# Optimization experiments

Hardware: AMD Instinct MI355X
Metric: run time of the kernel (lower is better)

The kernel has to match this reference:

```python
import jax, jax.numpy as jnp
import numpy as np

FEAT_DIM = 128
GUIDE_DIM = 128
NIR_DIM = 32
H_LR, W_LR = 128, 128
H_HR, W_HR = 256, 256
IMNET_IN = FEAT_DIM + 2 * GUIDE_DIM + 2  # 386


def make_coord_1d(n):
    # pixel-center coords in [-1, 1]: (2i+1)/n - 1
    return (2.0 * jnp.arange(n, dtype=jnp.float32) + 1.0) / n - 1.0


def nearest_sample(img, cy, cx):
    """F.grid_sample(img, grid, mode='nearest', align_corners=False, padding='zeros').
    img: [b, C, h, w]; cy, cx: [N] normalized coords (cy -> h axis, cx -> w axis).
    Returns sampled values [b, C, N] and the pixel-center coords (qcy, qcx) the
    nearest sample corresponds to (0 when out of range, matching zero padding)."""
    h, w = img.shape[-2], img.shape[-1]
    iy = jnp.round(((cy + 1.0) * h - 1.0) * 0.5).astype(jnp.int32)  # round-half-even == nearbyint
    ix = jnp.round(((cx + 1.0) * w - 1.0) * 0.5).astype(jnp.int32)
    valid = (iy >= 0) & (iy < h) & (ix >= 0) & (ix < w)
    iyc = jnp.clip(iy, 0, h - 1)
    ixc = jnp.clip(ix, 0, w - 1)
    out = img[:, :, iyc, ixc]                       # [b, C, N] gather
    out = jnp.where(valid[None, None, :], out, 0.0)
    qcy = jnp.where(valid, (2.0 * iyc.astype(jnp.float32) + 1.0) / h - 1.0, 0.0)
    qcx = jnp.where(valid, (2.0 * ixc.astype(jnp.float32) + 1.0) / w - 1.0, 0.0)
    return out, qcy, qcx


def mlp(x, W1, b1, W2, b2, W3, b3):
    x = jax.nn.relu(x @ W1 + b1)
    x = jax.nn.relu(x @ W2 + b2)
    return x @ W3 + b3


def setup_inputs() -> dict:
    key = jax.random.key(0)
    ks = jax.random.split(key, 9)
    return {
        "feat": jax.random.normal(ks[0], (1, FEAT_DIM, H_LR, W_LR), jnp.float32),
        "lr_guide": jax.random.normal(ks[1], (1, GUIDE_DIM, H_LR, W_LR), jnp.float32),
        "hr_guide": jax.random.normal(ks[2], (1, GUIDE_DIM, H_HR, W_HR), jnp.float32),
        "W1": jax.random.normal(ks[3], (IMNET_IN, 256), jnp.float32) * 0.05,
        "b1": jax.random.normal(ks[4], (256,), jnp.float32) * 0.05,
        "W2": jax.random.normal(ks[5], (256, 128), jnp.float32) * 0.05,
        "b2": jax.random.normal(ks[6], (128,), jnp.float32) * 0.05,
        "W3": jax.random.normal(ks[7], (128, NIR_DIM), jnp.float32) * 0.05,
        "b3": jax.random.normal(ks[8], (NIR_DIM,), jnp.float32) * 0.05,
    }


def reference(feat, lr_guide, hr_guide, W1, b1, W2, b2, W3, b3):
    b, _, h, w = feat.shape
    _, cg, H, W = hr_guide.shape
    N = H * W
    featc = jnp.concatenate([lr_guide, feat], axis=1)        # [b, guide+feat, h, w]

    gy, gx = jnp.meshgrid(make_coord_1d(H), make_coord_1d(W), indexing="ij")
    cy = gy.reshape(-1)                                      # [N] coord[:, 0] (h axis)
    cx = gx.reshape(-1)                                      # [N] coord[:, 1] (w axis)

    q_guide_hr = hr_guide.reshape(b, cg, N).transpose(0, 2, 1)  # [b, N, cg]

    # feat_ : gather at the unshifted coord (identical across neighbors)
    feat_b, _, _ = nearest_sample(featc, cy, cx)
    feat_b = feat_b.transpose(0, 2, 1)                       # [b, N, C]

    rx = 1.0 / h
    ry = 1.0 / w
    preds, gcs = [], []
    for vx in (-1.0, 1.0):
        for vy in (-1.0, 1.0):
            q_feat, qcy, qcx = nearest_sample(featc, cy + vx * rx, cx + vy * ry)
            q_feat = q_feat.transpose(0, 2, 1)               # [b, N, C]
            rel = jnp.stack([(cy - qcy) * h, (cx - qcx) * w], axis=-1)  # [N, 2]
            rel = jnp.broadcast_to(rel[None], (b, N, 2))
            inp = jnp.concatenate([q_feat, q_guide_hr, rel], axis=-1)  # [b, N, 386]
            preds.append(mlp(inp, W1, b1, W2, b2, W3, b3))   # [b, N, NIR]
            # bilateral color weight: dot over channels [-4:-1]
            gcs.append(jnp.sum(feat_b[..., -4:-1] * q_feat[..., -4:-1], axis=-1))
    preds = jnp.stack(preds, axis=-1)                        # [b, N, NIR, 4]
    weight = jax.nn.softmax(jnp.stack(gcs, axis=-1), axis=-1)  # [b, N, 4]
    ret = jnp.sum(preds * weight[:, :, None, :], axis=-1)    # [b, N, NIR]
    return ret.transpose(0, 2, 1).reshape(b, -1, H, W)
```

## Files before the change

kernel.cpp:

```cpp
#include <hip/hip_runtime.h>
#include <hip/hip_bf16.h>


using bf16x8 = __attribute__((ext_vector_type(8))) __bf16;
using f32x4  = __attribute__((ext_vector_type(4))) float;

__device__ __forceinline__ float bf2f(unsigned short u){
  unsigned int x = ((unsigned int)u) << 16;
  return __builtin_bit_cast(float, x);
}
__device__ __forceinline__ unsigned short f2bf(float f){
  unsigned int x = __builtin_bit_cast(unsigned int, f);
  unsigned int r = x + 0x7fffu + ((x >> 16) & 1u);
  return (unsigned short)(r >> 16);
}
__device__ __forceinline__ bf16x8 ld8(const ushort* p){
  uint4 r = *(const uint4*)p;
  return __builtin_bit_cast(bf16x8, r);
}

struct RowMeta { int valid, ix; float relY, relX; int spos; };
__device__ __forceinline__ RowMeta row_meta(int Y, int X, int br){
  int ivx = br >> 1, ivy = br & 1;
  int validY, iy; float relY;
  if (ivx == 0){ validY = (Y >= 1);   iy = (Y-1) >> 1; relY = (Y & 1) ?  0.5f :  1.5f; }
  else         { validY = (Y <= 254); iy = (Y+1) >> 1; relY = (Y & 1) ? -1.5f : -0.5f; }
  int validX, ix; float relX;
  if (ivy == 0){ validX = (X >= 1);   ix = (X-1) >> 1; relX = (X & 1) ?  0.5f :  1.5f; }
  else         { validX = (X <= 254); ix = (X+1) >> 1; relX = (X & 1) ? -1.5f : -0.5f; }
  RowMeta r;
  r.valid = validY && validX;
  r.ix = ix;
  if (r.valid){ r.relY = relY; r.relX = relX; r.spos = iy*128 + ix; }
  else { r.relY = (float)Y + 0.5f - 128.0f; r.relX = (float)X + 0.5f - 128.0f; r.spos = -1; }
  return r;
}

__global__ __launch_bounds__(256) void convert_weights(
    const float* __restrict__ W1, const float* __restrict__ b1,
    const float* __restrict__ W2, const float* __restrict__ W3,
    ushort* __restrict__ W1t,
    ushort* __restrict__ W2t,
    ushort* __restrict__ W3t,
    ushort* __restrict__ Ub)
{
  int b = blockIdx.x, t = threadIdx.x;
  if (b < 384){
    int i = b*256 + t;
    { int k = i >> 8, n = i & 255; W1t[n*384 + k] = f2bf(W1[i]); }
    if (i < 32768){ int k = i >> 7, n = i & 127; W2t[n*256 + k] = f2bf(W2[i]); }
    if (i < 4096) { int k = i >> 5, n = i & 31;  W3t[n*128 + k] = f2bf(W3[i]); }
  } else {
    int r = b - 384;
    float v = (r == 0) ? W1[384*256 + t] : (r == 1) ? W1[385*256 + t]
            : (r == 2) ? b1[t] : 0.0f;
    Ub[(size_t)(16384 + r)*256 + t] = f2bf(v);
  }
}

__global__ __launch_bounds__(256) void stage1_gemm(
    const float* __restrict__ src0, const float* __restrict__ src1,
    const ushort* __restrict__ W1t,
    ushort* __restrict__ outp)
{
  __shared__ ushort A[32*136];
  const int t = threadIdx.x;
  const int w = t >> 6, lane = t & 63, quad = lane >> 4, l15 = lane & 15;
  const int pos0  = (blockIdx.x >> 1) * 32;
  const int nside = (blockIdx.x & 1) * 128;
  const int mt = w >> 1;
  const int ntb = (w & 1) * 4;

  f32x4 acc[4];
  #pragma unroll
  for (int nt=0; nt<4; nt++) acc[nt] = f32x4{0.f,0.f,0.f,0.f};

  for (int h=0; h<2; h++){
    const float* src = h ? src1 : src0;
    #pragma unroll
    for (int i=0; i<16; i++){
      int f = i*256 + t;
      int k = f >> 5, mm = f & 31;
      A[mm*136 + k] = f2bf(src[(size_t)k*16384 + pos0 + mm]);
    }
    __syncthreads();
    #pragma unroll
    for (int kt=0; kt<4; kt++){
      bf16x8 a = ld8(&A[(mt*16 + l15)*136 + kt*32 + quad*8]);
      #pragma unroll
      for (int nt=0; nt<4; nt++){
        bf16x8 b = ld8(&W1t[(size_t)(nside + (ntb+nt)*16 + l15)*384 + h*128 + kt*32 + quad*8]);
        acc[nt] = __builtin_amdgcn_mfma_f32_16x16x32_bf16(a, b, acc[nt], 0,0,0);
      }
    }
    __syncthreads();
  }
  #pragma unroll
  for (int nt=0; nt<4; nt++){
    int n = nside + (ntb+nt)*16 + l15;
    #pragma unroll
    for (int r=0; r<4; r++){
      int mm = mt*16 + quad*4 + r;
      outp[(size_t)(pos0 + mm)*256 + n] = f2bf(acc[nt][r]);
    }
  }
}

__global__ __launch_bounds__(256, 4) void main_fused(
    const float* __restrict__ feat,
    const float* __restrict__ hr_guide,
    const float* __restrict__ b2v,
    const float* __restrict__ b3v,
    const ushort* __restrict__ Ub,
    const ushort* __restrict__ W1t,
    const ushort* __restrict__ W2t,
    const ushort* __restrict__ W3t,
    float* __restrict__ outp)
{
  __shared__ __align__(16) ushort A1[64*264];
  __shared__ __align__(16) ushort Ahr[16*136];
  __shared__ float gcs[64];
  __shared__ float wgt[64];

  const int t = threadIdx.x;
  const int w = t >> 6, lane = t & 63, quad = lane >> 4, l15 = lane & 15;
  const int Y  = blockIdx.x >> 4;
  const int X0 = (blockIdx.x & 15) << 4;
  const int iyA = (Y-1) >> 1, iyB = (Y+1) >> 1;
  const int ixbase = (X0-1) >> 1;

  #pragma unroll
  for (int i=0; i<2; i++){
    int id = i*256 + t;
    int ch = id >> 2, xq = id & 3;
    float4 v = *(const float4*)(hr_guide + (size_t)ch*65536 + Y*256 + X0 + xq*4);
    Ahr[(xq*4+0)*136 + ch] = f2bf(v.x);
    Ahr[(xq*4+1)*136 + ch] = f2bf(v.y);
    Ahr[(xq*4+2)*136 + ch] = f2bf(v.z);
    Ahr[(xq*4+3)*136 + ch] = f2bf(v.w);
  }
  if (t < 64){
    RowMeta g = row_meta(Y, X0 + (t>>2), t & 3);
    float gc = 0.0f;
    if (g.spos >= 0){
      int bpos = (Y>>1)*128 + ((X0 + (t>>2)) >> 1);
      #pragma unroll
      for (int cc=0; cc<3; cc++)
        gc += feat[(size_t)(124+cc)*16384 + bpos] * feat[(size_t)(124+cc)*16384 + g.spos];
    }
    gcs[t] = gc;
  }
  __syncthreads();
  if (t < 16){
    float g0 = gcs[t*4+0], g1 = gcs[t*4+1], g2 = gcs[t*4+2], g3 = gcs[t*4+3];
    float mx = fmaxf(fmaxf(g0,g1), fmaxf(g2,g3));
    float e0 = __expf(g0-mx), e1 = __expf(g1-mx), e2 = __expf(g2-mx), e3 = __expf(g3-mx);
    float inv = 1.0f/(e0+e1+e2+e3);
    wgt[t*4+0]=e0*inv; wgt[t*4+1]=e1*inv; wgt[t*4+2]=e2*inv; wgt[t*4+3]=e3*inv;
  }

  int uoff[8];
  #pragma unroll
  for (int j=0; j<8; j++){
    int s = quad*8 + j;
    int u = s - 3;
    int iy = (u < 10) ? iyA : iyB;
    int ix = ixbase + (u - ((u < 10) ? 0 : 10));
    iy = min(max(iy, 0), 127); ix = min(max(ix, 0), 127);
    int rid = iy*128 + ix;
    rid = (s == 0) ? 16384 : (s == 1) ? 16385 : (s == 2) ? 16386
        : (s >= 23) ? 16387 : rid;
    uoff[j] = rid * 256;
  }
  bf16x8 bk4[4];
  #pragma unroll
  for (int ct=0; ct<4; ct++){
    int m = 16*ct + l15;
    int pix = m >> 2, br = m & 3;
    RowMeta rm = row_meta(Y, X0 + pix, br);
    int sstar = rm.valid ? ((br >> 1)*10 + (rm.ix - ixbase) + 3) : -1;
    union { bf16x8 v; ushort s[8]; } bb;
    #pragma unroll
    for (int j=0; j<8; j++){
      int s = quad*8 + j;
      unsigned short val = 0;
      if (s == 0) val = f2bf(rm.relY);
      else if (s == 1) val = f2bf(rm.relX);
      else if (s == 2) val = 0x3F80u;
      if (s == sstar) val = 0x3F80u;
      bb.s[j] = val;
    }
    bk4[ct] = bb.v;
  }
  #pragma unroll
  for (int i=0; i<4; i++){
    int n = w*64 + i*16 + l15;
    const ushort* wp = W1t + (size_t)n*384 + 256;
    bf16x8 a0 = ld8(wp + 0*32 + quad*8);
    bf16x8 a1 = ld8(wp + 1*32 + quad*8);
    bf16x8 a2 = ld8(wp + 2*32 + quad*8);
    bf16x8 a3 = ld8(wp + 3*32 + quad*8);
    union { bf16x8 v; ushort s[8]; } a4;
    #pragma unroll
    for (int j=0; j<8; j++) a4.s[j] = Ub[(size_t)(uoff[j] + n)];
    #pragma unroll
    for (int ct=0; ct<4; ct++){
      const ushort* hp = &Ahr[(4*ct + (l15>>2))*136 + quad*8];
      f32x4 acc = f32x4{0.f,0.f,0.f,0.f};
      acc = __builtin_amdgcn_mfma_f32_16x16x32_bf16(a0, ld8(hp +  0), acc, 0,0,0);
      acc = __builtin_amdgcn_mfma_f32_16x16x32_bf16(a1, ld8(hp + 32), acc, 0,0,0);
      acc = __builtin_amdgcn_mfma_f32_16x16x32_bf16(a2, ld8(hp + 64), acc, 0,0,0);
      acc = __builtin_amdgcn_mfma_f32_16x16x32_bf16(a3, ld8(hp + 96), acc, 0,0,0);
      acc = __builtin_amdgcn_mfma_f32_16x16x32_bf16(a4.v, bk4[ct], acc, 0,0,0);
      int mrow = 16*ct + l15;
      int n0 = w*64 + i*16 + quad*4;
      uint2 o;
      o.x = (unsigned)f2bf(fmaxf(acc[0],0.f)) | ((unsigned)f2bf(fmaxf(acc[1],0.f)) << 16);
      o.y = (unsigned)f2bf(fmaxf(acc[2],0.f)) | ((unsigned)f2bf(fmaxf(acc[3],0.f)) << 16);
      *(uint2*)&A1[mrow*264 + n0] = o;
    }
  }
  __syncthreads();

  bf16x8 b2f[8][2];
  #pragma unroll
  for (int kt=0; kt<8; kt++)
    #pragma unroll
    for (int nt=0; nt<2; nt++)
      b2f[kt][nt] = ld8(&W2t[(size_t)(w*32 + nt*16 + l15)*256 + kt*32 + quad*8]);

  f32x4 acc2[4][2];
  #pragma unroll
  for (int mt=0; mt<4; mt++)
    #pragma unroll
    for (int nt=0; nt<2; nt++) acc2[mt][nt] = f32x4{0.f,0.f,0.f,0.f};
  #pragma unroll
  for (int mt=0; mt<4; mt++)
    #pragma unroll
    for (int kt=0; kt<8; kt++){
      bf16x8 a = ld8(&A1[(mt*16 + l15)*264 + kt*32 + quad*8]);
      #pragma unroll
      for (int nt=0; nt<2; nt++)
        acc2[mt][nt] = __builtin_amdgcn_mfma_f32_16x16x32_bf16(a, b2f[kt][nt], acc2[mt][nt], 0,0,0);
    }
  __syncthreads();

  {
    ushort* A2 = A1;
    float bias0 = b2v[w*32 + l15], bias1 = b2v[w*32 + 16 + l15];
    #pragma unroll
    for (int mt=0; mt<4; mt++)
      #pragma unroll
      for (int nt=0; nt<2; nt++){
        int n = w*32 + nt*16 + l15;
        float bv = nt ? bias1 : bias0;
        #pragma unroll
        for (int r=0; r<4; r++){
          int mm = mt*16 + quad*4 + r;
          A2[mm*136 + n] = f2bf(fmaxf(acc2[mt][nt][r] + bv, 0.0f));
        }
      }
  }
  __syncthreads();

  {
    bf16x8 b3f[4][2];
    #pragma unroll
    for (int kt=0; kt<4; kt++)
      #pragma unroll
      for (int nt=0; nt<2; nt++)
        b3f[kt][nt] = ld8(&W3t[(size_t)(nt*16 + l15)*128 + kt*32 + quad*8]);

    const ushort* A2 = A1;
    f32x4 acc3[2] = { f32x4{0.f,0.f,0.f,0.f}, f32x4{0.f,0.f,0.f,0.f} };
    #pragma unroll
    for (int kt=0; kt<4; kt++){
      bf16x8 a = ld8(&A2[(w*16 + l15)*136 + kt*32 + quad*8]);
      #pragma unroll
      for (int nt=0; nt<2; nt++)
        acc3[nt] = __builtin_amdgcn_mfma_f32_16x16x32_bf16(a, b3f[kt][nt], acc3[nt], 0,0,0);
    }
    int lp = w*4 + quad;
    int X = X0 + lp;
    float w0 = wgt[lp*4+0], w1 = wgt[lp*4+1], w2 = wgt[lp*4+2], w3 = wgt[lp*4+3];
    #pragma unroll
    for (int nt=0; nt<2; nt++){
      int n = nt*16 + l15;
      float bb = b3v[n];
      float v = w0*(acc3[nt][0]+bb) + w1*(acc3[nt][1]+bb)
              + w2*(acc3[nt][2]+bb) + w3*(acc3[nt][3]+bb);
      outp[(size_t)n*65536 + (size_t)Y*256 + X] = v;
    }
  }
}

extern "C" void kernel_launch(void* const* d_in, const int* in_sizes, int n_in,
                              void* d_out, int out_size, void* d_ws, size_t ws_size,
                              hipStream_t stream)
{
  const float* feat     = (const float*)d_in[0];
  const float* lr_guide = (const float*)d_in[1];
  const float* hr_guide = (const float*)d_in[2];
  const float* W1       = (const float*)d_in[3];
  const float* b1       = (const float*)d_in[4];
  const float* W2       = (const float*)d_in[5];
  const float* b2       = (const float*)d_in[6];
  const float* W3       = (const float*)d_in[7];
  const float* b3       = (const float*)d_in[8];
  float* outp = (float*)d_out;

  char* ws = (char*)d_ws;
  ushort* W1t = (ushort*)(ws);
  ushort* W2t = (ushort*)(ws + 196608);
  ushort* W3t = (ushort*)(ws + 196608 + 65536);
  ushort* Ub  = (ushort*)(ws + 196608 + 65536 + 8192);

  convert_weights<<<388, 256, 0, stream>>>(W1, b1, W2, W3, W1t, W2t, W3t, Ub);
  stage1_gemm<<<1024, 256, 0, stream>>>(lr_guide, feat, W1t, Ub);
  main_fused<<<4096, 256, 0, stream>>>(feat, hr_guide, b2, b3,
                                       Ub, W1t, W2t, W3t, outp);
}
```

Baseline: 207.8 us.

## Add precomputed U rows as epilogue bias instead of scattered MFMA gather

The per-row stage-1 result (U) is now loaded as contiguous uint2 vectors per output row and added in the layer-1 epilogue. This replaces the previous 8 scattered ushort gathers feeding a fifth MFMA with one-hot selectors. The rel/bias terms move to a small contiguous Wx table, and convert_weights is rewritten with coalesced reads and fewer blocks. W2/W3 fragment loads are hoisted earlier and split to overlap with layer-1 work, and the layer-2 loop order is swapped. These changes raise register pressure under the 4-blocks-per-SM launch bound.

```diff
diff --git a/kernel.cpp b/kernel.cpp
--- a/kernel.cpp
+++ b/kernel.cpp
@@ -42,19 +42,22 @@
     ushort* __restrict__ W1t,
     ushort* __restrict__ W2t,
     ushort* __restrict__ W3t,
-    ushort* __restrict__ Ub)
+    ushort* __restrict__ Wx,
+    ushort* __restrict__ Ubz)
 {
   int b = blockIdx.x, t = threadIdx.x;
-  if (b < 384){
-    int i = b*256 + t;
-    { int k = i >> 8, n = i & 255; W1t[n*384 + k] = f2bf(W1[i]); }
-    if (i < 32768){ int k = i >> 7, n = i & 127; W2t[n*256 + k] = f2bf(W2[i]); }
-    if (i < 4096) { int k = i >> 5, n = i & 31;  W3t[n*128 + k] = f2bf(W3[i]); }
+  if (b < 256){
+    W1t[b*384 + t] = f2bf(W1[t*256 + b]);
+    if (t < 128) W1t[b*384 + 256 + t] = f2bf(W1[(256+t)*256 + b]);
+    if (t < 32){
+      float v = (t==0) ? W1[384*256 + b] : (t==1) ? W1[385*256 + b]
+              : (t==2) ? b1[b] : 0.0f;
+      Wx[b*32 + t] = f2bf(v);
+    }
+    if (b < 128) W2t[b*256 + t] = f2bf(W2[t*128 + b]);
+    if (b < 32 && t < 128) W3t[b*128 + t] = f2bf(W3[t*32 + b]);
   } else {
-    int r = b - 384;
-    float v = (r == 0) ? W1[384*256 + t] : (r == 1) ? W1[385*256 + t]
-            : (r == 2) ? b1[t] : 0.0f;
-    Ub[(size_t)(16384 + r)*256 + t] = f2bf(v);
+    Ubz[t] = 0;
   }
 }
 
@@ -113,6 +116,7 @@
     const float* __restrict__ b3v,
     const ushort* __restrict__ Ub,
     const ushort* __restrict__ W1t,
+    const ushort* __restrict__ Wx,
     const ushort* __restrict__ W2t,
     const ushort* __restrict__ W3t,
     float* __restrict__ outp)
@@ -126,9 +130,18 @@
   const int w = t >> 6, lane = t & 63, quad = lane >> 4, l15 = lane & 15;
   const int Y  = blockIdx.x >> 4;
   const int X0 = (blockIdx.x & 15) << 4;
-  const int iyA = (Y-1) >> 1, iyB = (Y+1) >> 1;
-  const int ixbase = (X0-1) >> 1;
-
+
+  if (t < 64){
+    RowMeta g = row_meta(Y, X0 + (t>>2), t & 3);
+    float gc = 0.0f;
+    if (g.spos >= 0){
+      int bpos = (Y>>1)*128 + ((X0 + (t>>2)) >> 1);
+      #pragma unroll
+      for (int cc=0; cc<3; cc++)
+        gc += feat[(size_t)(124+cc)*16384 + bpos] * feat[(size_t)(124+cc)*16384 + g.spos];
+    }
+    gcs[t] = gc;
+  }
   #pragma unroll
   for (int i=0; i<2; i++){
     int id = i*256 + t;
@@ -139,16 +152,34 @@
     Ahr[(xq*4+2)*136 + ch] = f2bf(v.z);
     Ahr[(xq*4+3)*136 + ch] = f2bf(v.w);
   }
-  if (t < 64){
-    RowMeta g = row_meta(Y, X0 + (t>>2), t & 3);
-    float gc = 0.0f;
-    if (g.spos >= 0){
-      int bpos = (Y>>1)*128 + ((X0 + (t>>2)) >> 1);
-      #pragma unroll
-      for (int cc=0; cc<3; cc++)
-        gc += feat[(size_t)(124+cc)*16384 + bpos] * feat[(size_t)(124+cc)*16384 + g.spos];
-    }
-    gcs[t] = gc;
+  bf16x8 b2f[8][2];
+  #pragma unroll
+  for (int kt=0; kt<4; kt++)
+    #pragma unroll
+    for (int nt=0; nt<2; nt++)
+      b2f[kt][nt] = ld8(&W2t[(size_t)(w*32 + nt*16 + l15)*256 + kt*32 + quad*8]);
+
+  RowMeta rmct[4]; int urow[4];
+  #pragma unroll
+  for (int ct=0; ct<4; ct++){
+    int m = 16*ct + l15;
+    rmct[ct] = row_meta(Y, X0 + (m>>2), m & 3);
+    urow[ct] = rmct[ct].spos >= 0 ? rmct[ct].spos : 16387;
+  }
+  bf16x8 bk3[4];
+  #pragma unroll
+  for (int ct=0; ct<4; ct++){
+    union { bf16x8 v; ushort s[8]; } bb;
+    #pragma unroll
+    for (int j=0; j<8; j++){
+      int s = quad*8 + j;
+      unsigned short val = 0;
+      if (s == 0) val = f2bf(rmct[ct].relY);
+      else if (s == 1) val = f2bf(rmct[ct].relX);
+      else if (s == 2) val = 0x3F80u;
+      bb.s[j] = val;
+    }
+    bk3[ct] = bb.v;
   }
   __syncthreads();
   if (t < 16){
@@ -159,39 +190,6 @@
     wgt[t*4+0]=e0*inv; wgt[t*4+1]=e1*inv; wgt[t*4+2]=e2*inv; wgt[t*4+3]=e3*inv;
   }
 
-  int uoff[8];
-  #pragma unroll
-  for (int j=0; j<8; j++){
-    int s = quad*8 + j;
-    int u = s - 3;
-    int iy = (u < 10) ? iyA : iyB;
-    int ix = ixbase + (u - ((u < 10) ? 0 : 10));
-    iy = min(max(iy, 0), 127); ix = min(max(ix, 0), 127);
-    int rid = iy*128 + ix;
-    rid = (s == 0) ? 16384 : (s == 1) ? 16385 : (s == 2) ? 16386
-        : (s >= 23) ? 16387 : rid;
-    uoff[j] = rid * 256;
-  }
-  bf16x8 bk4[4];
-  #pragma unroll
-  for (int ct=0; ct<4; ct++){
-    int m = 16*ct + l15;
-    int pix = m >> 2, br = m & 3;
-    RowMeta rm = row_meta(Y, X0 + pix, br);
-    int sstar = rm.valid ? ((br >> 1)*10 + (rm.ix - ixbase) + 3) : -1;
-    union { bf16x8 v; ushort s[8]; } bb;
-    #pragma unroll
-    for (int j=0; j<8; j++){
-      int s = quad*8 + j;
-      unsigned short val = 0;
-      if (s == 0) val = f2bf(rm.relY);
-      else if (s == 1) val = f2bf(rm.relX);
-      else if (s == 2) val = 0x3F80u;
-      if (s == sstar) val = 0x3F80u;
-      bb.s[j] = val;
-    }
-    bk4[ct] = bb.v;
-  }
   #pragma unroll
   for (int i=0; i<4; i++){
     int n = w*64 + i*16 + l15;
@@ -200,9 +198,12 @@
     bf16x8 a1 = ld8(wp + 1*32 + quad*8);
     bf16x8 a2 = ld8(wp + 2*32 + quad*8);
     bf16x8 a3 = ld8(wp + 3*32 + quad*8);
-    union { bf16x8 v; ushort s[8]; } a4;
-    #pragma unroll
-    for (int j=0; j<8; j++) a4.s[j] = Ub[(size_t)(uoff[j] + n)];
+    bf16x8 a4 = ld8(&Wx[(size_t)n*32 + quad*8]);
+    int ncol0 = w*64 + i*16 + quad*4;
+    uint2 u4[4];
+    #pragma unroll
+    for (int ct=0; ct<4; ct++)
+      u4[ct] = *(const uint2*)&Ub[(size_t)urow[ct]*256 + ncol0];
     #pragma unroll
     for (int ct=0; ct<4; ct++){
       const ushort* hp = &Ahr[(4*ct + (l15>>2))*136 + quad*8];
@@ -211,20 +212,21 @@
       acc = __builtin_amdgcn_mfma_f32_16x16x32_bf16(a1, ld8(hp + 32), acc, 0,0,0);
       acc = __builtin_amdgcn_mfma_f32_16x16x32_bf16(a2, ld8(hp + 64), acc, 0,0,0);
       acc = __builtin_amdgcn_mfma_f32_16x16x32_bf16(a3, ld8(hp + 96), acc, 0,0,0);
-      acc = __builtin_amdgcn_mfma_f32_16x16x32_bf16(a4.v, bk4[ct], acc, 0,0,0);
+      acc = __builtin_amdgcn_mfma_f32_16x16x32_bf16(a4, bk3[ct], acc, 0,0,0);
+      union { uint2 v; ushort s[4]; } uu; uu.v = u4[ct];
       int mrow = 16*ct + l15;
-      int n0 = w*64 + i*16 + quad*4;
       uint2 o;
-      o.x = (unsigned)f2bf(fmaxf(acc[0],0.f)) | ((unsigned)f2bf(fmaxf(acc[1],0.f)) << 16);
-      o.y = (unsigned)f2bf(fmaxf(acc[2],0.f)) | ((unsigned)f2bf(fmaxf(acc[3],0.f)) << 16);
-      *(uint2*)&A1[mrow*264 + n0] = o;
+      o.x = (unsigned)f2bf(fmaxf(acc[0] + bf2f(uu.s[0]), 0.f))
+          | ((unsigned)f2bf(fmaxf(acc[1] + bf2f(uu.s[1]), 0.f)) << 16);
+      o.y = (unsigned)f2bf(fmaxf(acc[2] + bf2f(uu.s[2]), 0.f))
+          | ((unsigned)f2bf(fmaxf(acc[3] + bf2f(uu.s[3]), 0.f)) << 16);
+      *(uint2*)&A1[mrow*264 + ncol0] = o;
     }
   }
   __syncthreads();
 
-  bf16x8 b2f[8][2];
-  #pragma unroll
-  for (int kt=0; kt<8; kt++)
+  #pragma unroll
+  for (int kt=4; kt<8; kt++)
     #pragma unroll
     for (int nt=0; nt<2; nt++)
       b2f[kt][nt] = ld8(&W2t[(size_t)(w*32 + nt*16 + l15)*256 + kt*32 + quad*8]);
@@ -235,14 +237,21 @@
     #pragma unroll
     for (int nt=0; nt<2; nt++) acc2[mt][nt] = f32x4{0.f,0.f,0.f,0.f};
   #pragma unroll
-  for (int mt=0; mt<4; mt++)
-    #pragma unroll
-    for (int kt=0; kt<8; kt++){
+  for (int kt=0; kt<8; kt++)
+    #pragma unroll
+    for (int mt=0; mt<4; mt++){
       bf16x8 a = ld8(&A1[(mt*16 + l15)*264 + kt*32 + quad*8]);
       #pragma unroll
       for (int nt=0; nt<2; nt++)
         acc2[mt][nt] = __builtin_amdgcn_mfma_f32_16x16x32_bf16(a, b2f[kt][nt], acc2[mt][nt], 0,0,0);
     }
+
+  bf16x8 b3f[4][2];
+  #pragma unroll
+  for (int kt=0; kt<4; kt++)
+    #pragma unroll
+    for (int nt=0; nt<2; nt++)
+      b3f[kt][nt] = ld8(&W3t[(size_t)(nt*16 + l15)*128 + kt*32 + quad*8]);
   __syncthreads();
 
   {
@@ -264,13 +273,6 @@
   __syncthreads();
 
   {
-    bf16x8 b3f[4][2];
-    #pragma unroll
-    for (int kt=0; kt<4; kt++)
-      #pragma unroll
-      for (int nt=0; nt<2; nt++)
-        b3f[kt][nt] = ld8(&W3t[(size_t)(nt*16 + l15)*128 + kt*32 + quad*8]);
-
     const ushort* A2 = A1;
     f32x4 acc3[2] = { f32x4{0.f,0.f,0.f,0.f}, f32x4{0.f,0.f,0.f,0.f} };
     #pragma unroll
@@ -312,11 +314,13 @@
   char* ws = (char*)d_ws;
   ushort* W1t = (ushort*)(ws);
   ushort* W2t = (ushort*)(ws + 196608);
-  ushort* W3t = (ushort*)(ws + 196608 + 65536);
-  ushort* Ub  = (ushort*)(ws + 196608 + 65536 + 8192);
-
-  convert_weights<<<388, 256, 0, stream>>>(W1, b1, W2, W3, W1t, W2t, W3t, Ub);
+  ushort* W3t = (ushort*)(ws + 262144);
+  ushort* Wx  = (ushort*)(ws + 270336);
+  ushort* Ub  = (ushort*)(ws + 286720);
+  ushort* Ubz = Ub + (size_t)16387*256;
+
+  convert_weights<<<257, 256, 0, stream>>>(W1, b1, W2, W3, W1t, W2t, W3t, Wx, Ubz);
   stage1_gemm<<<1024, 256, 0, stream>>>(lr_guide, feat, W1t, Ub);
   main_fused<<<4096, 256, 0, stream>>>(feat, hr_guide, b2, b3,
-                                       Ub, W1t, W2t, W3t, outp);
-}
+                                       Ub, W1t, Wx, W2t, W3t, outp);
+}
```

Result: slower. 233.1 us (+12.1%).

## Shrink fused MLP tile to 8 pixels with two waves per block

Applied to the files above, without the earlier changes.

The fused per-pixel MLP kernel now processes 8 high-res pixels (32 branch rows) per 128-thread block instead of 16 pixels per 256 threads. Each wave covers a wider slice of the layer-1 and layer-2 outputs, and the gather window for low-res features is resized to match. The W3 fragment loads are moved ahead of a barrier. The weight conversion kernel is rewritten with fewer blocks and transposed indexing. Smaller blocks aim to raise occupancy and shrink shared memory, but every block now re-reads the same weight tiles for half as many pixels.

```diff
diff --git a/kernel.cpp b/kernel.cpp
--- a/kernel.cpp
+++ b/kernel.cpp
@@ -45,16 +45,17 @@
     ushort* __restrict__ Ub)
 {
   int b = blockIdx.x, t = threadIdx.x;
-  if (b < 384){
-    int i = b*256 + t;
-    { int k = i >> 8, n = i & 255; W1t[n*384 + k] = f2bf(W1[i]); }
-    if (i < 32768){ int k = i >> 7, n = i & 127; W2t[n*256 + k] = f2bf(W2[i]); }
-    if (i < 4096) { int k = i >> 5, n = i & 31;  W3t[n*128 + k] = f2bf(W3[i]); }
+  if (b < 256){
+    W1t[b*384 + t] = f2bf(W1[t*256 + b]);
+    if (t < 128) W1t[b*384 + 256 + t] = f2bf(W1[(256+t)*256 + b]);
+    if (b < 128) W2t[b*256 + t] = f2bf(W2[t*128 + b]);
+    if (b < 32 && t < 128) W3t[b*128 + t] = f2bf(W3[t*32 + b]);
   } else {
-    int r = b - 384;
-    float v = (r == 0) ? W1[384*256 + t] : (r == 1) ? W1[385*256 + t]
-            : (r == 2) ? b1[t] : 0.0f;
-    Ub[(size_t)(16384 + r)*256 + t] = f2bf(v);
+    ushort* U0 = Ub + (size_t)16384*256;
+    U0[t]       = f2bf(W1[384*256 + t]);
+    U0[256 + t] = f2bf(W1[385*256 + t]);
+    U0[512 + t] = f2bf(b1[t]);
+    U0[768 + t] = 0;
   }
 }
 
@@ -106,7 +107,7 @@
   }
 }
 
-__global__ __launch_bounds__(256, 4) void main_fused(
+__global__ __launch_bounds__(128, 4) void main_fused(
     const float* __restrict__ feat,
     const float* __restrict__ hr_guide,
     const float* __restrict__ b2v,
@@ -117,29 +118,29 @@
     const ushort* __restrict__ W3t,
     float* __restrict__ outp)
 {
-  __shared__ __align__(16) ushort A1[64*264];
-  __shared__ __align__(16) ushort Ahr[16*136];
-  __shared__ float gcs[64];
-  __shared__ float wgt[64];
+  __shared__ __align__(16) ushort A1[32*264];
+  __shared__ __align__(16) ushort Ahr[8*136];
+  __shared__ float gcs[32];
+  __shared__ float wgt[32];
 
   const int t = threadIdx.x;
   const int w = t >> 6, lane = t & 63, quad = lane >> 4, l15 = lane & 15;
-  const int Y  = blockIdx.x >> 4;
-  const int X0 = (blockIdx.x & 15) << 4;
+  const int Y  = blockIdx.x >> 5;
+  const int X0 = (blockIdx.x & 31) << 3;
   const int iyA = (Y-1) >> 1, iyB = (Y+1) >> 1;
   const int ixbase = (X0-1) >> 1;
 
   #pragma unroll
   for (int i=0; i<2; i++){
-    int id = i*256 + t;
-    int ch = id >> 2, xq = id & 3;
-    float4 v = *(const float4*)(hr_guide + (size_t)ch*65536 + Y*256 + X0 + xq*4);
-    Ahr[(xq*4+0)*136 + ch] = f2bf(v.x);
-    Ahr[(xq*4+1)*136 + ch] = f2bf(v.y);
-    Ahr[(xq*4+2)*136 + ch] = f2bf(v.z);
-    Ahr[(xq*4+3)*136 + ch] = f2bf(v.w);
-  }
-  if (t < 64){
+    int id = i*128 + t;
+    int ch = id >> 1, xh = id & 1;
+    float4 v = *(const float4*)(hr_guide + (size_t)ch*65536 + Y*256 + X0 + xh*4);
+    Ahr[(xh*4+0)*136 + ch] = f2bf(v.x);
+    Ahr[(xh*4+1)*136 + ch] = f2bf(v.y);
+    Ahr[(xh*4+2)*136 + ch] = f2bf(v.z);
+    Ahr[(xh*4+3)*136 + ch] = f2bf(v.w);
+  }
+  if (t < 32){
     RowMeta g = row_meta(Y, X0 + (t>>2), t & 3);
     float gc = 0.0f;
     if (g.spos >= 0){
@@ -151,7 +152,7 @@
     gcs[t] = gc;
   }
   __syncthreads();
-  if (t < 16){
+  if (t < 8){
     float g0 = gcs[t*4+0], g1 = gcs[t*4+1], g2 = gcs[t*4+2], g3 = gcs[t*4+3];
     float mx = fmaxf(fmaxf(g0,g1), fmaxf(g2,g3));
     float e0 = __expf(g0-mx), e1 = __expf(g1-mx), e2 = __expf(g2-mx), e3 = __expf(g3-mx);
@@ -164,22 +165,22 @@
   for (int j=0; j<8; j++){
     int s = quad*8 + j;
     int u = s - 3;
-    int iy = (u < 10) ? iyA : iyB;
-    int ix = ixbase + (u - ((u < 10) ? 0 : 10));
+    int iy = (u < 6) ? iyA : iyB;
+    int ix = ixbase + (u - ((u < 6) ? 0 : 6));
     iy = min(max(iy, 0), 127); ix = min(max(ix, 0), 127);
     int rid = iy*128 + ix;
     rid = (s == 0) ? 16384 : (s == 1) ? 16385 : (s == 2) ? 16386
-        : (s >= 23) ? 16387 : rid;
+        : (s >= 15) ? 16387 : rid;
     uoff[j] = rid * 256;
   }
-  bf16x8 bk4[4];
-  #pragma unroll
-  for (int ct=0; ct<4; ct++){
+  bf16x8 bk[2];
+  #pragma unroll
+  for (int ct=0; ct<2; ct++){
     int m = 16*ct + l15;
-    int pix = m >> 2, br = m & 3;
-    RowMeta rm = row_meta(Y, X0 + pix, br);
-    int sstar = rm.valid ? ((br >> 1)*10 + (rm.ix - ixbase) + 3) : -1;
-    union { bf16x8 v; ushort s[8]; } bb;
+    int br = m & 3;
+    RowMeta rm = row_meta(Y, X0 + (m>>2), br);
+    int sstar = rm.valid ? (3 + (br >> 1)*6 + (rm.ix - ixbase)) : -1;
+    union { bf16x8 v; ushort sh[8]; } bb;
     #pragma unroll
     for (int j=0; j<8; j++){
       int s = quad*8 + j;
@@ -188,72 +189,75 @@
       else if (s == 1) val = f2bf(rm.relX);
       else if (s == 2) val = 0x3F80u;
       if (s == sstar) val = 0x3F80u;
-      bb.s[j] = val;
-    }
-    bk4[ct] = bb.v;
-  }
-  #pragma unroll
-  for (int i=0; i<4; i++){
-    int n = w*64 + i*16 + l15;
+      bb.sh[j] = val;
+    }
+    bk[ct] = bb.v;
+  }
+  #pragma unroll 2
+  for (int i=0; i<8; i++){
+    int n = w*128 + i*16 + l15;
     const ushort* wp = W1t + (size_t)n*384 + 256;
     bf16x8 a0 = ld8(wp + 0*32 + quad*8);
     bf16x8 a1 = ld8(wp + 1*32 + quad*8);
     bf16x8 a2 = ld8(wp + 2*32 + quad*8);
     bf16x8 a3 = ld8(wp + 3*32 + quad*8);
-    union { bf16x8 v; ushort s[8]; } a4;
-    #pragma unroll
-    for (int j=0; j<8; j++) a4.s[j] = Ub[(size_t)(uoff[j] + n)];
-    #pragma unroll
-    for (int ct=0; ct<4; ct++){
+    union { bf16x8 v; ushort sh[8]; } a4;
+    #pragma unroll
+    for (int j=0; j<8; j++) a4.sh[j] = Ub[(size_t)(uoff[j] + n)];
+    int ncol0 = w*128 + i*16 + quad*4;
+    #pragma unroll
+    for (int ct=0; ct<2; ct++){
       const ushort* hp = &Ahr[(4*ct + (l15>>2))*136 + quad*8];
       f32x4 acc = f32x4{0.f,0.f,0.f,0.f};
       acc = __builtin_amdgcn_mfma_f32_16x16x32_bf16(a0, ld8(hp +  0), acc, 0,0,0);
       acc = __builtin_amdgcn_mfma_f32_16x16x32_bf16(a1, ld8(hp + 32), acc, 0,0,0);
       acc = __builtin_amdgcn_mfma_f32_16x16x32_bf16(a2, ld8(hp + 64), acc, 0,0,0);
       acc = __builtin_amdgcn_mfma_f32_16x16x32_bf16(a3, ld8(hp + 96), acc, 0,0,0);
-      acc = __builtin_amdgcn_mfma_f32_16x16x32_bf16(a4.v, bk4[ct], acc, 0,0,0);
+      acc = __builtin_amdgcn_mfma_f32_16x16x32_bf16(a4.v, bk[ct], acc, 0,0,0);
       int mrow = 16*ct + l15;
-      int n0 = w*64 + i*16 + quad*4;
       uint2 o;
       o.x = (unsigned)f2bf(fmaxf(acc[0],0.f)) | ((unsigned)f2bf(fmaxf(acc[1],0.f)) << 16);
       o.y = (unsigned)f2bf(fmaxf(acc[2],0.f)) | ((unsigned)f2bf(fmaxf(acc[3],0.f)) << 16);
-      *(uint2*)&A1[mrow*264 + n0] = o;
+      *(uint2*)&A1[mrow*264 + ncol0] = o;
     }
   }
   __syncthreads();
 
-  bf16x8 b2f[8][2];
-  #pragma unroll
-  for (int kt=0; kt<8; kt++)
+  f32x4 acc2[2][4];
+  #pragma unroll
+  for (int mt=0; mt<2; mt++)
+    #pragma unroll
+    for (int nt=0; nt<4; nt++) acc2[mt][nt] = f32x4{0.f,0.f,0.f,0.f};
+  #pragma unroll
+  for (int kt=0; kt<8; kt++){
+    bf16x8 bb[4];
+    #pragma unroll
+    for (int nt=0; nt<4; nt++)
+      bb[nt] = ld8(&W2t[(size_t)(w*64 + nt*16 + l15)*256 + kt*32 + quad*8]);
+    #pragma unroll
+    for (int mt=0; mt<2; mt++){
+      bf16x8 a = ld8(&A1[(mt*16 + l15)*264 + kt*32 + quad*8]);
+      #pragma unroll
+      for (int nt=0; nt<4; nt++)
+        acc2[mt][nt] = __builtin_amdgcn_mfma_f32_16x16x32_bf16(a, bb[nt], acc2[mt][nt], 0,0,0);
+    }
+  }
+  bf16x8 b3f[4][2];
+  #pragma unroll
+  for (int kt=0; kt<4; kt++)
     #pragma unroll
     for (int nt=0; nt<2; nt++)
-      b2f[kt][nt] = ld8(&W2t[(size_t)(w*32 + nt*16 + l15)*256 + kt*32 + quad*8]);
-
-  f32x4 acc2[4][2];
-  #pragma unroll
-  for (int mt=0; mt<4; mt++)
-    #pragma unroll
-    for (int nt=0; nt<2; nt++) acc2[mt][nt] = f32x4{0.f,0.f,0.f,0.f};
-  #pragma unroll
-  for (int mt=0; mt<4; mt++)
-    #pragma unroll
-    for (int kt=0; kt<8; kt++){
-      bf16x8 a = ld8(&A1[(mt*16 + l15)*264 + kt*32 + quad*8]);
-      #pragma unroll
-      for (int nt=0; nt<2; nt++)
-        acc2[mt][nt] = __builtin_amdgcn_mfma_f32_16x16x32_bf16(a, b2f[kt][nt], acc2[mt][nt], 0,0,0);
-    }
+      b3f[kt][nt] = ld8(&W3t[(size_t)(nt*16 + l15)*128 + kt*32 + quad*8]);
   __syncthreads();
 
   {
     ushort* A2 = A1;
-    float bias0 = b2v[w*32 + l15], bias1 = b2v[w*32 + 16 + l15];
-    #pragma unroll
-    for (int mt=0; mt<4; mt++)
-      #pragma unroll
-      for (int nt=0; nt<2; nt++){
-        int n = w*32 + nt*16 + l15;
-        float bv = nt ? bias1 : bias0;
+    #pragma unroll
+    for (int mt=0; mt<2; mt++)
+      #pragma unroll
+      for (int nt=0; nt<4; nt++){
+        int n = w*64 + nt*16 + l15;
+        float bv = b2v[n];
         #pragma unroll
         for (int r=0; r<4; r++){
           int mm = mt*16 + quad*4 + r;
@@ -264,13 +268,6 @@
   __syncthreads();
 
   {
-    bf16x8 b3f[4][2];
-    #pragma unroll
-    for (int kt=0; kt<4; kt++)
-      #pragma unroll
-      for (int nt=0; nt<2; nt++)
-        b3f[kt][nt] = ld8(&W3t[(size_t)(nt*16 + l15)*128 + kt*32 + quad*8]);
-
     const ushort* A2 = A1;
     f32x4 acc3[2] = { f32x4{0.f,0.f,0.f,0.f}, f32x4{0.f,0.f,0.f,0.f} };
     #pragma unroll
@@ -312,11 +309,11 @@
   char* ws = (char*)d_ws;
   ushort* W1t = (ushort*)(ws);
   ushort* W2t = (ushort*)(ws + 196608);
-  ushort* W3t = (ushort*)(ws + 196608 + 65536);
-  ushort* Ub  = (ushort*)(ws + 196608 + 65536 + 8192);
-
-  convert_weights<<<388, 256, 0, stream>>>(W1, b1, W2, W3, W1t, W2t, W3t, Ub);
+  ushort* W3t = (ushort*)(ws + 262144);
+  ushort* Ub  = (ushort*)(ws + 270336);
+
+  convert_weights<<<257, 256, 0, stream>>>(W1, b1, W2, W3, W1t, W2t, W3t, Ub);
   stage1_gemm<<<1024, 256, 0, stream>>>(lr_guide, feat, W1t, Ub);
-  main_fused<<<4096, 256, 0, stream>>>(feat, hr_guide, b2, b3,
+  main_fused<<<8192, 128, 0, stream>>>(feat, hr_guide, b2, b3,
                                        Ub, W1t, W2t, W3t, outp);
 }
```

After: 272.1 us. +31.0%, slower.
